# Kernel optimization log

Hardware: AMD Instinct MI355X
Metric: run time of the kernel (lower is better)

## Reference

```python
import jax, jax.numpy as jnp
import numpy as np

NUM_PARAMS = 8  # number of trainable RY gates (module __init__ default)
BATCH = 1000000
N_WIRES = 4


def _apply_ry(state, theta, wire):
    """Apply RY(theta) on `wire`. state: (B,2,2,2,2) real; theta: scalar or (B,).
    RY = [[cos(t/2), -sin(t/2)], [sin(t/2), cos(t/2)]] (real)."""
    axis = wire + 1
    half = theta * 0.5
    c, s = jnp.cos(half), jnp.sin(half)
    s0 = jax.lax.index_in_dim(state, 0, axis, keepdims=False)  # (B,2,2,2)
    s1 = jax.lax.index_in_dim(state, 1, axis, keepdims=False)
    # broadcast per-batch angles over remaining qubit axes
    c = jnp.reshape(c, c.shape + (1,) * (s0.ndim - c.ndim))
    s = jnp.reshape(s, s.shape + (1,) * (s0.ndim - s.ndim))
    new0 = c * s0 - s * s1
    new1 = s * s0 + c * s1
    return jnp.stack([new0, new1], axis=axis)


def _apply_cnot(state, control, target):
    """Apply CNOT(control, target): flip target amplitudes where control=1."""
    ca, ta = control + 1, target + 1
    c0 = jax.lax.index_in_dim(state, 0, ca, keepdims=False)
    c1 = jax.lax.index_in_dim(state, 1, ca, keepdims=False)
    ta2 = ta - 1 if ta > ca else ta  # target axis shifts after control axis removed
    c1 = jnp.flip(c1, axis=ta2)
    return jnp.stack([c0, c1], axis=ca)


def setup_inputs() -> dict:
    key = jax.random.key(0)
    k1, k2 = jax.random.split(key)
    inputs = jax.random.normal(k1, (BATCH, N_WIRES), dtype=jnp.float32)
    weights = jax.random.normal(k2, (NUM_PARAMS,), dtype=jnp.float32)
    return {"inputs": inputs, "weights": weights}


def reference(inputs, weights):
    B = inputs.shape[0]
    # |0000> initial state, batched
    state = jnp.zeros((B, 2, 2, 2, 2), dtype=inputs.dtype).at[:, 0, 0, 0, 0].set(1.0)
    # data encoding: RY(inputs[:, w]) on wire w
    for w in range(N_WIRES):
        state = _apply_ry(state, inputs[:, w], w)
    # variational layer
    for i in range(NUM_PARAMS):
        state = _apply_ry(state, weights[i], i % N_WIRES)
        state = _apply_cnot(state, i % N_WIRES, (i + 1) % N_WIRES)
    # <Z_w> = p(wire w = 0) - p(wire w = 1); state is real so probs = state**2
    probs = state * state
    outs = []
    for w in range(N_WIRES):
        other_axes = tuple(a for a in range(1, N_WIRES + 1) if a != w + 1)
        p = probs.sum(axis=other_axes)  # (B, 2)
        outs.append(p[:, 0] - p[:, 1])
    return jnp.stack(outs, axis=1)  # (B, 4)
```

## Files before the change

kernel.cpp:

```cpp
#include <hip/hip_runtime.h>


__global__ __launch_bounds__(256) void qpe_kernel(
    const float* __restrict__ inputs,
    const float* __restrict__ weights,
    float* __restrict__ out,
    int B)
{
    int b = blockIdx.x * blockDim.x + threadIdx.x;
    if (b >= B) return;

    float cw[8], sw[8];
#pragma unroll
    for (int i = 0; i < 8; ++i) {
        float h = weights[i] * 0.5f;
        __sincosf(h, &sw[i], &cw[i]);
    }

    float4 x = *reinterpret_cast<const float4*>(inputs + (size_t)b * 4);
    float c[4], s[4];
    __sincosf(x.x * 0.5f, &s[0], &c[0]);
    __sincosf(x.y * 0.5f, &s[1], &c[1]);
    __sincosf(x.z * 0.5f, &s[2], &c[2]);
    __sincosf(x.w * 0.5f, &s[3], &c[3]);

    float amp[16];
#pragma unroll
    for (int idx = 0; idx < 16; ++idx) {
        float a = ((idx >> 3) & 1) ? s[0] : c[0];
        a *= ((idx >> 2) & 1) ? s[1] : c[1];
        a *= ((idx >> 1) & 1) ? s[2] : c[2];
        a *= ( idx       & 1) ? s[3] : c[3];
        amp[idx] = a;
    }

#pragma unroll
    for (int i = 0; i < 8; ++i) {
        const int q  = i & 3;
        const int t  = (i + 1) & 3;
        const int qm = 1 << (3 - q);
        const int tm = 1 << (3 - t);
        const float ci = cw[i], si = sw[i];
#pragma unroll
        for (int idx = 0; idx < 16; ++idx) {
            if (idx & qm) continue;
            float a0 = amp[idx], a1 = amp[idx | qm];
            amp[idx]      = ci * a0 - si * a1;
            amp[idx | qm] = si * a0 + ci * a1;
        }
#pragma unroll
        for (int idx = 0; idx < 16; ++idx) {
            if (!(idx & qm) || (idx & tm)) continue;
            float tmp = amp[idx];
            amp[idx]      = amp[idx | tm];
            amp[idx | tm] = tmp;
        }
    }

    float p[16];
#pragma unroll
    for (int idx = 0; idx < 16; ++idx) p[idx] = amp[idx] * amp[idx];

    float z[4];
#pragma unroll
    for (int w = 0; w < 4; ++w) {
        const int m = 1 << (3 - w);
        float acc = 0.0f;
#pragma unroll
        for (int idx = 0; idx < 16; ++idx)
            acc += (idx & m) ? -p[idx] : p[idx];
        z[w] = acc;
    }

    *reinterpret_cast<float4*>(out + (size_t)b * 4) = make_float4(z[0], z[1], z[2], z[3]);
}

extern "C" void kernel_launch(void* const* d_in, const int* in_sizes, int n_in,
                              void* d_out, int out_size, void* d_ws, size_t ws_size,
                              hipStream_t stream) {
    const float* inputs  = (const float*)d_in[0];
    const float* weights = (const float*)d_in[1];
    float* out = (float*)d_out;
    const int B = in_sizes[0] / 4;

    const int block = 256;
    const int grid  = (B + block - 1) / block;
    qpe_kernel<<<grid, block, 0, stream>>>(inputs, weights, out, B);
}
```

Baseline: 17.81 us.

## Pack amplitudes into float2 vectors and process four batch items per thread

The 16-amplitude state is stored as eight 2-wide vectors so the compiler can emit packed FP32 math (v_pk_fma). Wire-3 rotations become intra-vector mixes, and CNOTs become register swaps. Each thread now handles four batch elements with a grid stride, which amortises the weight sincos across them. The reduction is rewritten as pairwise vector sums. The risk is that fewer threads reduce memory-level parallelism on a bandwidth-bound kernel.

Result: faster. 15.51 us (-12.9%).

```diff
diff --git a/kernel.cpp b/kernel.cpp
--- a/kernel.cpp
+++ b/kernel.cpp
@@ -1,5 +1,7 @@
 #include <hip/hip_runtime.h>
 
+
+typedef float v2f __attribute__((ext_vector_type(2)));
 
 __global__ __launch_bounds__(256) void qpe_kernel(
     const float* __restrict__ inputs,
@@ -7,72 +9,103 @@
     float* __restrict__ out,
     int B)
 {
-    int b = blockIdx.x * blockDim.x + threadIdx.x;
-    if (b >= B) return;
+    const int tid = blockIdx.x * blockDim.x + threadIdx.x;
+    const int S   = gridDim.x * blockDim.x;
 
     float cw[8], sw[8];
 #pragma unroll
     for (int i = 0; i < 8; ++i) {
         float h = weights[i] * 0.5f;
-        __sincosf(h, &sw[i], &cw[i]);
-    }
-
-    float4 x = *reinterpret_cast<const float4*>(inputs + (size_t)b * 4);
-    float c[4], s[4];
-    __sincosf(x.x * 0.5f, &s[0], &c[0]);
-    __sincosf(x.y * 0.5f, &s[1], &c[1]);
-    __sincosf(x.z * 0.5f, &s[2], &c[2]);
-    __sincosf(x.w * 0.5f, &s[3], &c[3]);
-
-    float amp[16];
-#pragma unroll
-    for (int idx = 0; idx < 16; ++idx) {
-        float a = ((idx >> 3) & 1) ? s[0] : c[0];
-        a *= ((idx >> 2) & 1) ? s[1] : c[1];
-        a *= ((idx >> 1) & 1) ? s[2] : c[2];
-        a *= ( idx       & 1) ? s[3] : c[3];
-        amp[idx] = a;
+        sw[i] = __sinf(h);
+        cw[i] = __cosf(h);
     }
 
 #pragma unroll
-    for (int i = 0; i < 8; ++i) {
-        const int q  = i & 3;
-        const int t  = (i + 1) & 3;
-        const int qm = 1 << (3 - q);
-        const int tm = 1 << (3 - t);
-        const float ci = cw[i], si = sw[i];
+    for (int j = 0; j < 4; ++j) {
+        const int b = tid + j * S;
+        if (b >= B) continue;
+
+        float4 x = *reinterpret_cast<const float4*>(inputs + (size_t)b * 4);
+        float c0 = __cosf(x.x * 0.5f), s0 = __sinf(x.x * 0.5f);
+        float c1 = __cosf(x.y * 0.5f), s1 = __sinf(x.y * 0.5f);
+        float c2 = __cosf(x.z * 0.5f), s2 = __sinf(x.z * 0.5f);
+        float c3 = __cosf(x.w * 0.5f), s3 = __sinf(x.w * 0.5f);
+
+        const v2f e3 = {c3, s3};
+        float f01[4];
+        f01[0] = c0 * c1; f01[1] = c0 * s1; f01[2] = s0 * c1; f01[3] = s0 * s1;
+        v2f amp[8];
 #pragma unroll
-        for (int idx = 0; idx < 16; ++idx) {
-            if (idx & qm) continue;
-            float a0 = amp[idx], a1 = amp[idx | qm];
-            amp[idx]      = ci * a0 - si * a1;
-            amp[idx | qm] = si * a0 + ci * a1;
+        for (int k = 0; k < 8; ++k) {
+            float p = f01[k >> 1] * ((k & 1) ? s2 : c2);
+            amp[k] = p * e3;
         }
+
 #pragma unroll
-        for (int idx = 0; idx < 16; ++idx) {
-            if (!(idx & qm) || (idx & tm)) continue;
-            float tmp = amp[idx];
-            amp[idx]      = amp[idx | tm];
-            amp[idx | tm] = tmp;
+        for (int i = 0; i < 8; ++i) {
+            const int q = i & 3;
+            const float ci = cw[i], si = sw[i];
+            if (q < 3) {
+                const int m2 = 1 << (2 - q);
+#pragma unroll
+                for (int k = 0; k < 8; ++k) {
+                    if (k & m2) continue;
+                    v2f a0 = amp[k], a1 = amp[k | m2];
+                    amp[k]      = ci * a0 - si * a1;
+                    amp[k | m2] = si * a0 + ci * a1;
+                }
+            } else {
+                const v2f sv = {-si, si};
+#pragma unroll
+                for (int k = 0; k < 8; ++k) {
+                    v2f a = amp[k];
+                    v2f sp = {a.y, a.x};
+                    amp[k] = ci * a + sv * sp;
+                }
+            }
+            if (q == 0) {
+                v2f t4 = amp[4]; amp[4] = amp[6]; amp[6] = t4;
+                v2f t5 = amp[5]; amp[5] = amp[7]; amp[7] = t5;
+            } else if (q == 1) {
+                v2f t2 = amp[2]; amp[2] = amp[3]; amp[3] = t2;
+                v2f t6 = amp[6]; amp[6] = amp[7]; amp[7] = t6;
+            } else if (q == 2) {
+#pragma unroll
+                for (int k = 1; k < 8; k += 2) {
+                    v2f a = amp[k];
+                    amp[k] = (v2f){a.y, a.x};
+                }
+            } else {
+#pragma unroll
+                for (int k = 0; k < 4; ++k) {
+                    v2f lo = amp[k], hi = amp[k | 4];
+                    amp[k]     = (v2f){lo.x, hi.y};
+                    amp[k | 4] = (v2f){hi.x, lo.y};
+                }
+            }
         }
+
+        v2f sq[8];
+#pragma unroll
+        for (int k = 0; k < 8; ++k) sq[k] = amp[k] * amp[k];
+
+        v2f a01 = sq[0] + sq[1], a23 = sq[2] + sq[3];
+        v2f a45 = sq[4] + sq[5], a67 = sq[6] + sq[7];
+        v2f b0123 = a01 + a23, b4567 = a45 + a67;
+        v2f z0v = b0123 - b4567;
+        v2f z1v = (a01 + a45) - (a23 + a67);
+        v2f ce = (sq[0] + sq[2]) + (sq[4] + sq[6]);
+        v2f co = (sq[1] + sq[3]) + (sq[5] + sq[7]);
+        v2f z2v = ce - co;
+        v2f tot = b0123 + b4567;
+
+        float4 z;
+        z.x = z0v.x + z0v.y;
+        z.y = z1v.x + z1v.y;
+        z.z = z2v.x + z2v.y;
+        z.w = tot.x - tot.y;
+        *reinterpret_cast<float4*>(out + (size_t)b * 4) = z;
     }
-
-    float p[16];
-#pragma unroll
-    for (int idx = 0; idx < 16; ++idx) p[idx] = amp[idx] * amp[idx];
-
-    float z[4];
-#pragma unroll
-    for (int w = 0; w < 4; ++w) {
-        const int m = 1 << (3 - w);
-        float acc = 0.0f;
-#pragma unroll
-        for (int idx = 0; idx < 16; ++idx)
-            acc += (idx & m) ? -p[idx] : p[idx];
-        z[w] = acc;
-    }
-
-    *reinterpret_cast<float4*>(out + (size_t)b * 4) = make_float4(z[0], z[1], z[2], z[3]);
 }
 
 extern "C" void kernel_launch(void* const* d_in, const int* in_sizes, int n_in,
@@ -84,6 +117,8 @@
     const int B = in_sizes[0] / 4;
 
     const int block = 256;
-    const int grid  = (B + block - 1) / block;
+    const int elems_per_thread = 4;
+    const int threads = (B + elems_per_thread - 1) / elems_per_thread;
+    const int grid = (threads + block - 1) / block;
     qpe_kernel<<<grid, block, 0, stream>>>(inputs, weights, out, B);
 }
```
